# Performance work log

Measured on AMD Instinct MI355X. Metric: run time of the kernel, lower is better.

Reference implementation:

```python
import jax, jax.numpy as jnp
import numpy as np

WINDOW = 16  # signature_window_size
D = 6        # input_path_dim


def _mlp(x, Ws, bs, final_act):
    for W, b in zip(Ws[:-1], bs[:-1]):
        x = jax.nn.softplus(W @ x + b)
    return final_act(Ws[-1] @ x + bs[-1])


def _windowed_logsig(xs):
    """Depth-2 log-signature of each window of the (piecewise-linear) path.
    Returns level-1 increments [n, D] and Levy areas [n, D, D] (antisymmetric)."""
    dx = xs[1:] - xs[:-1]                              # [T-1, D]
    n = dx.shape[0] // WINDOW
    dxw = dx[: n * WINDOW].reshape(n, WINDOW, D)
    lvl1 = dxw.sum(axis=1)                             # [n, D]
    cum = jnp.cumsum(dxw, axis=1) - dxw                # exclusive prefix sums
    cross = jnp.einsum('nwi,nwj->nij', cum, dxw)
    area = 0.5 * (cross - jnp.swapaxes(cross, 1, 2))   # [n, D, D]
    return lvl1, area


def setup_inputs() -> dict:
    key = jax.random.key(0)
    ks = jax.random.split(key, 9)
    S, H, OUT = 128, 128, 10
    B, T = 8, 513

    def lin(k, o, i):
        return jax.random.normal(k, (o, i), jnp.float32) / np.sqrt(i)

    return {
        'x': jax.random.normal(ks[0], (B, T, D), jnp.float32),
        'W_i0': lin(ks[1], H, D), 'b_i0': jnp.zeros((H,), jnp.float32),
        'W_i1': lin(ks[2], H, H), 'b_i1': jnp.zeros((H,), jnp.float32),
        'W_i2': lin(ks[3], S, H), 'b_i2': jnp.zeros((S,), jnp.float32),
        'W_v0': lin(ks[4], H, S), 'b_v0': jnp.zeros((H,), jnp.float32),
        'W_v1': lin(ks[5], H, H), 'b_v1': jnp.zeros((H,), jnp.float32),
        'W_v2': lin(ks[6], D * S, H), 'b_v2': jnp.zeros((D * S,), jnp.float32),
        'W_r': lin(ks[7], OUT, S), 'b_r': jnp.zeros((OUT,), jnp.float32),
    }


def reference(x, W_i0, b_i0, W_i1, b_i1, W_i2, b_i2,
              W_v0, b_v0, W_v1, b_v1, W_v2, b_v2, W_r, b_r):
    S = W_i2.shape[0]
    init_mlp = lambda z: _mlp(z, (W_i0, W_i1, W_i2), (b_i0, b_i1, b_i2), lambda u: u)
    # Vector fields V_i: R^S -> R^S, one per input channel (split_multi_vector_field)
    vf = lambda h: _mlp(h, (W_v0, W_v1, W_v2), (b_v0, b_v1, b_v2), jnp.tanh).reshape(D, S)
    mask = jnp.triu(jnp.ones((D, D), x.dtype), 1)  # Lyndon words i<j at depth 2

    def single(xs):  # xs: [T, D]
        lvl1, area = _windowed_logsig(xs)
        h0 = init_mlp(xs[0])

        def step(h, sig):
            l1, a = sig
            V = vf(h)                                  # [D, S]
            J = jax.jacfwd(vf)(h)                      # [D, S, S], J[j,b,a]=dV_j[b]/dh[a]
            M = jnp.einsum('jba,ia->ijb', J, V)        # (DV_j)(h) V_i(h)
            brack = M - jnp.swapaxes(M, 0, 1)          # Lie brackets [V_i, V_j](h)
            h_new = h + jnp.einsum('i,ib->b', l1, V) \
                      + jnp.einsum('ij,ijb->b', a * mask, brack)  # log-ODE step
            return h_new, h_new

        _, hist = jax.lax.scan(step, h0, (lvl1, area))
        hist = jnp.concatenate([h0[None], hist], axis=0)   # [n+1, S]
        return hist @ W_r.T + b_r                          # evolving readout

    return jax.vmap(single)(x)
```

## Files before the change

kernel.cpp:

```cpp
#include <hip/hip_runtime.h>
#include <math.h>

#define D    6
#define S    128
#define H    128
#define WIN  16
#define BB   8
#define TT   513
#define NW   32
#define OUTD 10

__device__ float g_lvl1[BB * NW * D];
__device__ float g_area[BB * NW * D * D];
__device__ float g_h0[BB * S];
__device__ float g_hist[BB * (NW + 1) * S];

__device__ __forceinline__ float sp(float x) {
    return (x > 20.f) ? x : log1pf(expf(x));
}
__device__ __forceinline__ float sigm(float x) {
    return 1.f / (1.f + expf(-x));
}
__device__ __forceinline__ float dot4(float4 a, float4 b, float acc) {
    return fmaf(a.x, b.x, fmaf(a.y, b.y, fmaf(a.z, b.z, fmaf(a.w, b.w, acc))));
}

#define O_W0   0
#define O_W1   16384
#define O_PS   32768
#define O_U    35840
#define O_T    36608
#define O_V    37376
#define O_H    38144
#define O_U1   38400
#define O_U2   38528
#define O_SG1  38656
#define O_SG2  38784
#define O_B0   38912
#define O_B1   39040
#define O_SIG  39168
#define SMTOT  39256

__global__ __launch_bounds__(256) void k_sig(
        const float* __restrict__ x,
        const float* __restrict__ Wi0, const float* __restrict__ bi0,
        const float* __restrict__ Wi1, const float* __restrict__ bi1,
        const float* __restrict__ Wi2, const float* __restrict__ bi2) {
    const int b = blockIdx.x;
    const int tid = threadIdx.x;
    __shared__ float dxs[NW][WIN][D];
    __shared__ float cums[NW][WIN][D];
    __shared__ float ua[H], ub[H];

    const float* xb = x + (size_t)b * TT * D;

    if (tid < NW * D) {
        int w = tid / D, i = tid % D;
        float run = 0.f;
        float prev = xb[(w * WIN) * D + i];
        for (int k = 0; k < WIN; ++k) {
            float cur = xb[(w * WIN + k + 1) * D + i];
            float d = cur - prev; prev = cur;
            dxs[w][k][i] = d;
            cums[w][k][i] = run;
            run += d;
        }
        g_lvl1[(b * NW + w) * D + i] = run;
    }
    __syncthreads();
    for (int e = tid; e < NW * D * D; e += blockDim.x) {
        int w = e / (D * D); int rem = e % (D * D);
        int i = rem / D, j = rem % D;
        float s = 0.f;
        for (int k = 0; k < WIN; ++k)
            s += cums[w][k][i] * dxs[w][k][j] - cums[w][k][j] * dxs[w][k][i];
        g_area[(b * NW + w) * (D * D) + rem] = 0.5f * s;
    }
    if (tid < H) {
        float z = bi0[tid];
        for (int k = 0; k < D; ++k) z += Wi0[tid * D + k] * xb[k];
        ua[tid] = sp(z);
    }
    __syncthreads();
    if (tid < H) {
        float z = bi1[tid];
        for (int k = 0; k < H; ++k) z += Wi1[tid * H + k] * ua[k];
        ub[tid] = sp(z);
    }
    __syncthreads();
    if (tid < H) {
        float z = bi2[tid];
        for (int k = 0; k < H; ++k) z += Wi2[tid * H + k] * ub[k];
        g_h0[b * S + tid] = z;
    }
}

#define FOR16(X) X(0) X(1) X(2) X(3) X(4) X(5) X(6) X(7) \
                 X(8) X(9) X(10) X(11) X(12) X(13) X(14) X(15)
#define DECL_ABC(q) float4 wA##q, wB##q, wC##q;
#define LOAD_ABC(q) wA##q = W24[baseA + q]; wB##q = W24[baseB + q]; wC##q = W24[baseC + q];
#define S3_Q(q) { float4 u = U24[q]; \
    acc0 = dot4(wA##q, u, acc0); acc1 = dot4(wB##q, u, acc1); acc2 = dot4(wC##q, u, acc2); }
#define S6_Q(q) { \
    acc0 = dot4(wA##q, TA[q], acc0); acc1 = dot4(wB##q, TB[q], acc1); acc2 = dot4(wC##q, TC[q], acc2); }

__global__ __launch_bounds__(512, 2) void k_scan(
        const float* __restrict__ bv0, const float* __restrict__ bv1,
        const float* __restrict__ bv2,
        const float* __restrict__ Wv0, const float* __restrict__ Wv1,
        const float* __restrict__ Wv2) {
    __shared__ float sm[SMTOT];
    const int b = blockIdx.x, tid = threadIdx.x;
    const int r   = tid & 127;
    const int c4  = tid >> 7;
    const int key = r & 7;
    const int kh = tid & 1;
    const int r0 = tid >> 1, r1 = r0 + 256, r2 = r0 + 512;
    const int jA = tid >> 8, jB = 2 + jA, jC = 4 + jA;

    {
        float4* d = (float4*)(sm + O_W0);
        const float4* s0 = (const float4*)Wv0;
        const float4* s1 = (const float4*)Wv1;
        for (int i = tid; i < 4096; i += 512) { d[i] = s0[i]; d[4096 + i] = s1[i]; }
    }
    FOR16(DECL_ABC)
    const float4* W24 = (const float4*)Wv2;
    const int baseA = r0 * 32 + kh * 16;
    const int baseB = r1 * 32 + kh * 16;
    const int baseC = r2 * 32 + kh * 16;
    FOR16(LOAD_ABC)
    if (tid < 128) {
        sm[O_B0 + tid] = bv0[tid]; sm[O_B1 + tid] = bv1[tid];
        float h0v = g_h0[b * 128 + tid];
        sm[O_H + tid] = h0v;
        g_hist[(b * (NW + 1)) * 128 + tid] = h0v;
    }
    if (tid >= 448) {
        int q = tid - 448;
        if (q < 42)
            sm[O_SIG + q] = (q < 6) ? g_lvl1[(b * NW) * 6 + q]
                                    : g_area[(b * NW) * 36 + q - 6];
    }
    __syncthreads();

    const float4* W04 = (const float4*)(sm + O_W0);
    const float4* W14 = (const float4*)(sm + O_W1);

    int p = 0;
    for (int t = 0; t < NW; ++t) {
        float rsig = 0.f;
        if (tid >= 448) {
            int q = tid - 448;
            if (q < 42 && t + 1 < NW)
                rsig = (q < 6) ? g_lvl1[(b * NW + t + 1) * 6 + q]
                               : g_area[(b * NW + t + 1) * 36 + q - 6];
        }
        const int sb = O_SIG + (t & 1) * 44;

        {
            float a = 0.f;
            const float4* H4 = (const float4*)(sm + O_H + p * 128);
            #pragma unroll
            for (int q = 0; q < 8; ++q) {
                int qq = c4 * 8 + (q ^ key);
                a = dot4(W04[r * 32 + qq], H4[qq], a);
            }
            sm[O_PS + (c4 * 6) * 128 + r] = a;
        }
        __syncthreads();
        if (tid < 128) {
            float z = sm[O_B0 + tid];
            #pragma unroll
            for (int c = 0; c < 4; ++c) z += sm[O_PS + (c * 6) * 128 + tid];
            sm[O_U1 + tid] = sp(z); sm[O_SG1 + tid] = sigm(z);
        }
        __syncthreads();
        {
            float a = 0.f;
            const float4* U14 = (const float4*)(sm + O_U1);
            #pragma unroll
            for (int q = 0; q < 8; ++q) {
                int qq = c4 * 8 + (q ^ key);
                a = dot4(W14[r * 32 + qq], U14[qq], a);
            }
            sm[O_PS + (c4 * 6) * 128 + r] = a;
        }
        __syncthreads();
        if (tid < 128) {
            float z = sm[O_B1 + tid];
            #pragma unroll
            for (int c = 0; c < 4; ++c) z += sm[O_PS + (c * 6) * 128 + tid];
            sm[O_U2 + tid] = sp(z); sm[O_SG2 + tid] = sigm(z);
        }
        __syncthreads();
        {
            float acc0 = 0.f, acc1 = 0.f, acc2 = 0.f;
            const float4* U24 = (const float4*)(sm + O_U2) + kh * 16;
            FOR16(S3_Q)
            sm[O_PS + kh * 768 + r0] = acc0;
            sm[O_PS + kh * 768 + r1] = acc1;
            sm[O_PS + kh * 768 + r2] = acc2;
        }
        __syncthreads();
        {
            sm[O_V + tid] = tanhf(bv2[tid] + sm[O_PS + tid] + sm[O_PS + 768 + tid]);
            if (tid < 256) {
                int e = tid + 512;
                sm[O_V + e] = tanhf(bv2[e] + sm[O_PS + e] + sm[O_PS + 768 + e]);
            }
        }
        __syncthreads();
        {
            #pragma unroll
            for (int s = 0; s < 2; ++s) {
                int e = tid + s * 512;
                if (s == 0 || tid < 256) {
                    int jj = e >> 7, rr = e & 127;
                    float u = 0.f;
                    #pragma unroll
                    for (int i = 0; i < 6; ++i)
                        u = fmaf(sm[sb + 6 + i * 6 + jj], sm[O_V + i * 128 + rr], u);
                    sm[O_U + jj * 128 + rr] = u;
                }
            }
            if (tid < 128) {
                float xh = sm[O_H + p * 128 + tid];
                #pragma unroll
                for (int i = 0; i < 6; ++i)
                    xh = fmaf(sm[sb + i], sm[O_V + i * 128 + tid], xh);
                sm[O_H + (p ^ 1) * 128 + tid] = xh;
            }
        }
        __syncthreads();
        {
            float a0 = 0.f, a1 = 0.f, a2 = 0.f, a3 = 0.f, a4 = 0.f, a5 = 0.f;
            const float4* U4 = (const float4*)(sm + O_U);
            #pragma unroll
            for (int q = 0; q < 8; ++q) {
                int qq = c4 * 8 + (q ^ key);
                float4 w = W04[r * 32 + qq];
                a0 = dot4(w, U4[qq], a0);
                a1 = dot4(w, U4[32 + qq], a1);
                a2 = dot4(w, U4[64 + qq], a2);
                a3 = dot4(w, U4[96 + qq], a3);
                a4 = dot4(w, U4[128 + qq], a4);
                a5 = dot4(w, U4[160 + qq], a5);
            }
            sm[O_PS + (c4 * 6 + 0) * 128 + r] = a0;
            sm[O_PS + (c4 * 6 + 1) * 128 + r] = a1;
            sm[O_PS + (c4 * 6 + 2) * 128 + r] = a2;
            sm[O_PS + (c4 * 6 + 3) * 128 + r] = a3;
            sm[O_PS + (c4 * 6 + 4) * 128 + r] = a4;
            sm[O_PS + (c4 * 6 + 5) * 128 + r] = a5;
        }
        __syncthreads();
        {
            #pragma unroll
            for (int s = 0; s < 2; ++s) {
                int e = tid + s * 512;
                if (s == 0 || tid < 256) {
                    int jj = e >> 7, rr = e & 127;
                    float sv = sm[O_PS + jj * 128 + rr] + sm[O_PS + (6 + jj) * 128 + rr]
                             + sm[O_PS + (12 + jj) * 128 + rr] + sm[O_PS + (18 + jj) * 128 + rr];
                    sm[O_T + jj * 128 + rr] = sm[O_SG1 + rr] * sv;
                }
            }
        }
        __syncthreads();
        {
            float a0 = 0.f, a1 = 0.f, a2 = 0.f, a3 = 0.f, a4 = 0.f, a5 = 0.f;
            const float4* T4 = (const float4*)(sm + O_T);
            #pragma unroll
            for (int q = 0; q < 8; ++q) {
                int qq = c4 * 8 + (q ^ key);
                float4 w = W14[r * 32 + qq];
                a0 = dot4(w, T4[qq], a0);
                a1 = dot4(w, T4[32 + qq], a1);
                a2 = dot4(w, T4[64 + qq], a2);
                a3 = dot4(w, T4[96 + qq], a3);
                a4 = dot4(w, T4[128 + qq], a4);
                a5 = dot4(w, T4[160 + qq], a5);
            }
            sm[O_PS + (c4 * 6 + 0) * 128 + r] = a0;
            sm[O_PS + (c4 * 6 + 1) * 128 + r] = a1;
            sm[O_PS + (c4 * 6 + 2) * 128 + r] = a2;
            sm[O_PS + (c4 * 6 + 3) * 128 + r] = a3;
            sm[O_PS + (c4 * 6 + 4) * 128 + r] = a4;
            sm[O_PS + (c4 * 6 + 5) * 128 + r] = a5;
        }
        __syncthreads();
        {
            #pragma unroll
            for (int s = 0; s < 2; ++s) {
                int e = tid + s * 512;
                if (s == 0 || tid < 256) {
                    int jj = e >> 7, rr = e & 127;
                    float sv = sm[O_PS + jj * 128 + rr] + sm[O_PS + (6 + jj) * 128 + rr]
                             + sm[O_PS + (12 + jj) * 128 + rr] + sm[O_PS + (18 + jj) * 128 + rr];
                    sm[O_U + jj * 128 + rr] = sm[O_SG2 + rr] * sv;
                }
            }
        }
        __syncthreads();
        {
            float acc0 = 0.f, acc1 = 0.f, acc2 = 0.f;
            const float4* TA = (const float4*)(sm + O_U) + jA * 32 + kh * 16;
            const float4* TB = (const float4*)(sm + O_U) + jB * 32 + kh * 16;
            const float4* TC = (const float4*)(sm + O_U) + jC * 32 + kh * 16;
            FOR16(S6_Q)
            sm[O_PS + kh * 768 + r0] = acc0;
            sm[O_PS + kh * 768 + r1] = acc1;
            sm[O_PS + kh * 768 + r2] = acc2;
        }
        __syncthreads();
        {
            float v = sm[O_V + tid];
            sm[O_T + tid] = (1.f - v * v) * (sm[O_PS + tid] + sm[O_PS + 768 + tid]);
            if (tid < 256) {
                int e = tid + 512;
                float v2 = sm[O_V + e];
                sm[O_T + e] = (1.f - v2 * v2) * (sm[O_PS + e] + sm[O_PS + 768 + e]);
            }
        }
        __syncthreads();
        if (tid < 128) {
            float xh = sm[O_H + (p ^ 1) * 128 + tid];
            #pragma unroll
            for (int j = 0; j < 6; ++j) xh += sm[O_T + j * 128 + tid];
            sm[O_H + (p ^ 1) * 128 + tid] = xh;
            g_hist[(b * (NW + 1) + t + 1) * 128 + tid] = xh;
        }
        if (tid >= 448) {
            int q = tid - 448;
            if (q < 42 && t + 1 < NW)
                sm[O_SIG + ((t + 1) & 1) * 44 + q] = rsig;
        }
        p ^= 1;
        __syncthreads();
    }
}

__global__ __launch_bounds__(384) void k_read(const float* __restrict__ Wr,
                                              const float* __restrict__ br,
                                              float* __restrict__ out) {
    const int b = blockIdx.x, e = threadIdx.x;
    if (e < (NW + 1) * OUTD) {
        int t = e / OUTD, o = e % OUTD;
        float z = br[o];
        const float4* hrow = (const float4*)&g_hist[(b * (NW + 1) + t) * 128];
        const float4* wrow = (const float4*)&Wr[o * 128];
        float z0 = 0, z1 = 0, z2 = 0, z3 = 0;
        #pragma unroll 8
        for (int s4 = 0; s4 < 32; ++s4) {
            float4 hv = hrow[s4]; float4 wv = wrow[s4];
            z0 = fmaf(hv.x, wv.x, z0); z1 = fmaf(hv.y, wv.y, z1);
            z2 = fmaf(hv.z, wv.z, z2); z3 = fmaf(hv.w, wv.w, z3);
        }
        out[(b * (NW + 1) + t) * OUTD + o] = z + ((z0 + z1) + (z2 + z3));
    }
}

extern "C" void kernel_launch(void* const* d_in, const int* in_sizes, int n_in,
                              void* d_out, int out_size, void* d_ws, size_t ws_size,
                              hipStream_t stream) {
    const float* x   = (const float*)d_in[0];
    const float* Wi0 = (const float*)d_in[1];
    const float* bi0 = (const float*)d_in[2];
    const float* Wi1 = (const float*)d_in[3];
    const float* bi1 = (const float*)d_in[4];
    const float* Wi2 = (const float*)d_in[5];
    const float* bi2 = (const float*)d_in[6];
    const float* Wv0 = (const float*)d_in[7];
    const float* bv0 = (const float*)d_in[8];
    const float* Wv1 = (const float*)d_in[9];
    const float* bv1 = (const float*)d_in[10];
    const float* Wv2 = (const float*)d_in[11];
    const float* bv2 = (const float*)d_in[12];
    const float* Wr  = (const float*)d_in[13];
    const float* br  = (const float*)d_in[14];
    float* out = (float*)d_out;

    hipLaunchKernelGGL(k_sig,  dim3(BB), dim3(256), 0, stream,
                       x, Wi0, bi0, Wi1, bi1, Wi2, bi2);
    hipLaunchKernelGGL(k_scan, dim3(BB), dim3(512), 0, stream,
                       bv0, bv1, bv2, Wv0, Wv1, Wv2);
    hipLaunchKernelGGL(k_read, dim3(BB), dim3(384), 0, stream, Wr, br, out);
}
```

Before: 476.5 us.

## Replace shared-memory partial sums with wavefront shuffle reductions to cut barriers in scan

Reworks the per-step matvecs in the scan kernel so each output row is reduced across 4 or 2 adjacent lanes with shuffles instead of writing partials to shared memory and reducing in a separate phase. This removes about five barrier-separated phases per time step and fuses the activations (softplus/sigmoid/tanh, tanh derivative) into the reduction epilogue. Two-thirds of the Wv2 register cache is dropped in favour of global/L2 reads each step, and launch bounds no longer request 2 blocks per CU. The tradeoff is extra global loads for Wv2 rows in exchange for lower register pressure and fewer syncs.

```diff
diff --git a/kernel.cpp b/kernel.cpp
--- a/kernel.cpp
+++ b/kernel.cpp
@@ -27,19 +27,19 @@
 
 #define O_W0   0
 #define O_W1   16384
-#define O_PS   32768
-#define O_U    35840
-#define O_T    36608
-#define O_V    37376
-#define O_H    38144
-#define O_U1   38400
-#define O_U2   38528
-#define O_SG1  38656
-#define O_SG2  38784
-#define O_B0   38912
-#define O_B1   39040
-#define O_SIG  39168
-#define SMTOT  39256
+#define O_U1   32768
+#define O_SG1  32896
+#define O_U2   33024
+#define O_SG2  33152
+#define O_V    33280
+#define O_U    34048
+#define O_TB   34816
+#define O_H    35584
+#define O_B0   35840
+#define O_B1   35968
+#define O_B2   36096
+#define O_SIG  36864
+#define SMTOT  36952
 
 __global__ __launch_bounds__(256) void k_sig(
         const float* __restrict__ x,
@@ -97,39 +97,50 @@
 
 #define FOR16(X) X(0) X(1) X(2) X(3) X(4) X(5) X(6) X(7) \
                  X(8) X(9) X(10) X(11) X(12) X(13) X(14) X(15)
-#define DECL_ABC(q) float4 wA##q, wB##q, wC##q;
-#define LOAD_ABC(q) wA##q = W24[baseA + q]; wB##q = W24[baseB + q]; wC##q = W24[baseC + q];
-#define S3_Q(q) { float4 u = U24[q]; \
-    acc0 = dot4(wA##q, u, acc0); acc1 = dot4(wB##q, u, acc1); acc2 = dot4(wC##q, u, acc2); }
-#define S6_Q(q) { \
-    acc0 = dot4(wA##q, TA[q], acc0); acc1 = dot4(wB##q, TB[q], acc1); acc2 = dot4(wC##q, TC[q], acc2); }
-
-__global__ __launch_bounds__(512, 2) void k_scan(
+#define DECL_A(q) float4 wA##q;
+#define LOAD_A(q) wA##q = W24[baseA + q];
+#define C_Q(q) { float4 u = U24[q]; \
+    acc0 = dot4(wA##q, u, acc0); \
+    acc1 = dot4(Wm1[q], u, acc1); \
+    acc2 = dot4(Wm2[q], u, acc2); }
+#define G_Q(q) { \
+    acc0 = dot4(wA##q, TA[q], acc0); \
+    acc1 = dot4(Wm1[q], TJB[q], acc1); \
+    acc2 = dot4(Wm2[q], TJC[q], acc2); }
+
+__global__ __launch_bounds__(512) void k_scan(
         const float* __restrict__ bv0, const float* __restrict__ bv1,
         const float* __restrict__ bv2,
         const float* __restrict__ Wv0, const float* __restrict__ Wv1,
         const float* __restrict__ Wv2) {
     __shared__ float sm[SMTOT];
     const int b = blockIdx.x, tid = threadIdx.x;
-    const int r   = tid & 127;
-    const int c4  = tid >> 7;
-    const int key = r & 7;
+    const int r   = tid >> 2;
+    const int sub = tid & 3;
+    const int keyA = r & 7;
     const int kh = tid & 1;
-    const int r0 = tid >> 1, r1 = r0 + 256, r2 = r0 + 512;
-    const int jA = tid >> 8, jB = 2 + jA, jC = 4 + jA;
+    const int m  = tid >> 1;
+    const int rp = tid >> 3, jg = (tid >> 2) & 1, kq = tid & 3;
+    const int ra = 2 * rp, rb = ra + 1, j0 = 3 * jg;
+    const int keyE = rp & 7;
 
     {
         float4* d = (float4*)(sm + O_W0);
         const float4* s0 = (const float4*)Wv0;
         const float4* s1 = (const float4*)Wv1;
-        for (int i = tid; i < 4096; i += 512) { d[i] = s0[i]; d[4096 + i] = s1[i]; }
-    }
-    FOR16(DECL_ABC)
+        #pragma unroll
+        for (int i = 0; i < 8; ++i) { d[tid + i * 512] = s0[tid + i * 512]; }
+        #pragma unroll
+        for (int i = 0; i < 8; ++i) { d[4096 + tid + i * 512] = s1[tid + i * 512]; }
+        sm[O_B2 + tid] = bv2[tid];
+        if (tid < 256) sm[O_B2 + 512 + tid] = bv2[512 + tid];
+    }
+    FOR16(DECL_A)
     const float4* W24 = (const float4*)Wv2;
-    const int baseA = r0 * 32 + kh * 16;
-    const int baseB = r1 * 32 + kh * 16;
-    const int baseC = r2 * 32 + kh * 16;
-    FOR16(LOAD_ABC)
+    const int baseA = m * 32 + kh * 16;
+    FOR16(LOAD_A)
+    const float4* Wm1 = W24 + (m + 256) * 32 + kh * 16;
+    const float4* Wm2 = W24 + (m + 512) * 32 + kh * 16;
     if (tid < 128) {
         sm[O_B0 + tid] = bv0[tid]; sm[O_B1 + tid] = bv1[tid];
         float h0v = g_h0[b * 128 + tid];
@@ -159,55 +170,51 @@
         const int sb = O_SIG + (t & 1) * 44;
 
         {
-            float a = 0.f;
+            float a0 = 0.f, a1 = 0.f;
             const float4* H4 = (const float4*)(sm + O_H + p * 128);
             #pragma unroll
-            for (int q = 0; q < 8; ++q) {
-                int qq = c4 * 8 + (q ^ key);
-                a = dot4(W04[r * 32 + qq], H4[qq], a);
-            }
-            sm[O_PS + (c4 * 6) * 128 + r] = a;
-        }
-        __syncthreads();
-        if (tid < 128) {
-            float z = sm[O_B0 + tid];
-            #pragma unroll
-            for (int c = 0; c < 4; ++c) z += sm[O_PS + (c * 6) * 128 + tid];
-            sm[O_U1 + tid] = sp(z); sm[O_SG1 + tid] = sigm(z);
-        }
-        __syncthreads();
-        {
-            float a = 0.f;
+            for (int q = 0; q < 8; q += 2) {
+                int q0 = sub * 8 + (q ^ keyA);
+                int q1 = sub * 8 + ((q + 1) ^ keyA);
+                a0 = dot4(W04[r * 32 + q0], H4[q0], a0);
+                a1 = dot4(W04[r * 32 + q1], H4[q1], a1);
+            }
+            float tot = a0 + a1;
+            tot += __shfl_xor(tot, 1);
+            tot += __shfl_xor(tot, 2);
+            if (sub == 0)      sm[O_U1 + r]  = sp(sm[O_B0 + r] + tot);
+            else if (sub == 1) sm[O_SG1 + r] = sigm(sm[O_B0 + r] + tot);
+        }
+        __syncthreads();
+        {
+            float a0 = 0.f, a1 = 0.f;
             const float4* U14 = (const float4*)(sm + O_U1);
             #pragma unroll
-            for (int q = 0; q < 8; ++q) {
-                int qq = c4 * 8 + (q ^ key);
-                a = dot4(W14[r * 32 + qq], U14[qq], a);
-            }
-            sm[O_PS + (c4 * 6) * 128 + r] = a;
-        }
-        __syncthreads();
-        if (tid < 128) {
-            float z = sm[O_B1 + tid];
-            #pragma unroll
-            for (int c = 0; c < 4; ++c) z += sm[O_PS + (c * 6) * 128 + tid];
-            sm[O_U2 + tid] = sp(z); sm[O_SG2 + tid] = sigm(z);
+            for (int q = 0; q < 8; q += 2) {
+                int q0 = sub * 8 + (q ^ keyA);
+                int q1 = sub * 8 + ((q + 1) ^ keyA);
+                a0 = dot4(W14[r * 32 + q0], U14[q0], a0);
+                a1 = dot4(W14[r * 32 + q1], U14[q1], a1);
+            }
+            float tot = a0 + a1;
+            tot += __shfl_xor(tot, 1);
+            tot += __shfl_xor(tot, 2);
+            if (sub == 0)      sm[O_U2 + r]  = sp(sm[O_B1 + r] + tot);
+            else if (sub == 1) sm[O_SG2 + r] = sigm(sm[O_B1 + r] + tot);
         }
         __syncthreads();
         {
             float acc0 = 0.f, acc1 = 0.f, acc2 = 0.f;
             const float4* U24 = (const float4*)(sm + O_U2) + kh * 16;
-            FOR16(S3_Q)
-            sm[O_PS + kh * 768 + r0] = acc0;
-            sm[O_PS + kh * 768 + r1] = acc1;
-            sm[O_PS + kh * 768 + r2] = acc2;
-        }
-        __syncthreads();
-        {
-            sm[O_V + tid] = tanhf(bv2[tid] + sm[O_PS + tid] + sm[O_PS + 768 + tid]);
-            if (tid < 256) {
-                int e = tid + 512;
-                sm[O_V + e] = tanhf(bv2[e] + sm[O_PS + e] + sm[O_PS + 768 + e]);
+            FOR16(C_Q)
+            acc0 += __shfl_xor(acc0, 1);
+            acc1 += __shfl_xor(acc1, 1);
+            acc2 += __shfl_xor(acc2, 1);
+            if (kh == 0) {
+                sm[O_V + m]       = tanhf(sm[O_B2 + m] + acc0);
+                sm[O_V + m + 256] = tanhf(sm[O_B2 + m + 256] + acc1);
+            } else {
+                sm[O_V + m + 512] = tanhf(sm[O_B2 + m + 512] + acc2);
             }
         }
         __syncthreads();
@@ -234,100 +241,90 @@
         }
         __syncthreads();
         {
-            float a0 = 0.f, a1 = 0.f, a2 = 0.f, a3 = 0.f, a4 = 0.f, a5 = 0.f;
+            float aa0=0,aa1=0,aa2=0, ab0=0,ab1=0,ab2=0;
             const float4* U4 = (const float4*)(sm + O_U);
             #pragma unroll
             for (int q = 0; q < 8; ++q) {
-                int qq = c4 * 8 + (q ^ key);
-                float4 w = W04[r * 32 + qq];
-                a0 = dot4(w, U4[qq], a0);
-                a1 = dot4(w, U4[32 + qq], a1);
-                a2 = dot4(w, U4[64 + qq], a2);
-                a3 = dot4(w, U4[96 + qq], a3);
-                a4 = dot4(w, U4[128 + qq], a4);
-                a5 = dot4(w, U4[160 + qq], a5);
-            }
-            sm[O_PS + (c4 * 6 + 0) * 128 + r] = a0;
-            sm[O_PS + (c4 * 6 + 1) * 128 + r] = a1;
-            sm[O_PS + (c4 * 6 + 2) * 128 + r] = a2;
-            sm[O_PS + (c4 * 6 + 3) * 128 + r] = a3;
-            sm[O_PS + (c4 * 6 + 4) * 128 + r] = a4;
-            sm[O_PS + (c4 * 6 + 5) * 128 + r] = a5;
-        }
-        __syncthreads();
-        {
-            #pragma unroll
-            for (int s = 0; s < 2; ++s) {
-                int e = tid + s * 512;
-                if (s == 0 || tid < 256) {
-                    int jj = e >> 7, rr = e & 127;
-                    float sv = sm[O_PS + jj * 128 + rr] + sm[O_PS + (6 + jj) * 128 + rr]
-                             + sm[O_PS + (12 + jj) * 128 + rr] + sm[O_PS + (18 + jj) * 128 + rr];
-                    sm[O_T + jj * 128 + rr] = sm[O_SG1 + rr] * sv;
-                }
-            }
-        }
-        __syncthreads();
-        {
-            float a0 = 0.f, a1 = 0.f, a2 = 0.f, a3 = 0.f, a4 = 0.f, a5 = 0.f;
-            const float4* T4 = (const float4*)(sm + O_T);
+                int qq = kq * 8 + (q ^ keyE);
+                float4 wa = W04[ra * 32 + qq], wb = W04[rb * 32 + qq];
+                float4 u0 = U4[j0 * 32 + qq], u1 = U4[(j0+1) * 32 + qq], u2 = U4[(j0+2) * 32 + qq];
+                aa0 = dot4(wa, u0, aa0); aa1 = dot4(wa, u1, aa1); aa2 = dot4(wa, u2, aa2);
+                ab0 = dot4(wb, u0, ab0); ab1 = dot4(wb, u1, ab1); ab2 = dot4(wb, u2, ab2);
+            }
+            aa0 += __shfl_xor(aa0,1); aa0 += __shfl_xor(aa0,2);
+            aa1 += __shfl_xor(aa1,1); aa1 += __shfl_xor(aa1,2);
+            aa2 += __shfl_xor(aa2,1); aa2 += __shfl_xor(aa2,2);
+            ab0 += __shfl_xor(ab0,1); ab0 += __shfl_xor(ab0,2);
+            ab1 += __shfl_xor(ab1,1); ab1 += __shfl_xor(ab1,2);
+            ab2 += __shfl_xor(ab2,1); ab2 += __shfl_xor(ab2,2);
+            if (kq == 0) {
+                float sg = sm[O_SG1 + ra];
+                sm[O_TB + j0 * 128 + ra] = sg * aa0;
+                sm[O_TB + (j0+1) * 128 + ra] = sg * aa1;
+                sm[O_TB + (j0+2) * 128 + ra] = sg * aa2;
+            } else if (kq == 1) {
+                float sg = sm[O_SG1 + rb];
+                sm[O_TB + j0 * 128 + rb] = sg * ab0;
+                sm[O_TB + (j0+1) * 128 + rb] = sg * ab1;
+                sm[O_TB + (j0+2) * 128 + rb] = sg * ab2;
+            }
+        }
+        __syncthreads();
+        {
+            float aa0=0,aa1=0,aa2=0, ab0=0,ab1=0,ab2=0;
+            const float4* T4 = (const float4*)(sm + O_TB);
             #pragma unroll
             for (int q = 0; q < 8; ++q) {
-                int qq = c4 * 8 + (q ^ key);
-                float4 w = W14[r * 32 + qq];
-                a0 = dot4(w, T4[qq], a0);
-                a1 = dot4(w, T4[32 + qq], a1);
-                a2 = dot4(w, T4[64 + qq], a2);
-                a3 = dot4(w, T4[96 + qq], a3);
-                a4 = dot4(w, T4[128 + qq], a4);
-                a5 = dot4(w, T4[160 + qq], a5);
-            }
-            sm[O_PS + (c4 * 6 + 0) * 128 + r] = a0;
-            sm[O_PS + (c4 * 6 + 1) * 128 + r] = a1;
-            sm[O_PS + (c4 * 6 + 2) * 128 + r] = a2;
-            sm[O_PS + (c4 * 6 + 3) * 128 + r] = a3;
-            sm[O_PS + (c4 * 6 + 4) * 128 + r] = a4;
-            sm[O_PS + (c4 * 6 + 5) * 128 + r] = a5;
-        }
-        __syncthreads();
-        {
-            #pragma unroll
-            for (int s = 0; s < 2; ++s) {
-                int e = tid + s * 512;
-                if (s == 0 || tid < 256) {
-                    int jj = e >> 7, rr = e & 127;
-                    float sv = sm[O_PS + jj * 128 + rr] + sm[O_PS + (6 + jj) * 128 + rr]
-                             + sm[O_PS + (12 + jj) * 128 + rr] + sm[O_PS + (18 + jj) * 128 + rr];
-                    sm[O_U + jj * 128 + rr] = sm[O_SG2 + rr] * sv;
-                }
+                int qq = kq * 8 + (q ^ keyE);
+                float4 wa = W14[ra * 32 + qq], wb = W14[rb * 32 + qq];
+                float4 u0 = T4[j0 * 32 + qq], u1 = T4[(j0+1) * 32 + qq], u2 = T4[(j0+2) * 32 + qq];
+                aa0 = dot4(wa, u0, aa0); aa1 = dot4(wa, u1, aa1); aa2 = dot4(wa, u2, aa2);
+                ab0 = dot4(wb, u0, ab0); ab1 = dot4(wb, u1, ab1); ab2 = dot4(wb, u2, ab2);
+            }
+            aa0 += __shfl_xor(aa0,1); aa0 += __shfl_xor(aa0,2);
+            aa1 += __shfl_xor(aa1,1); aa1 += __shfl_xor(aa1,2);
+            aa2 += __shfl_xor(aa2,1); aa2 += __shfl_xor(aa2,2);
+            ab0 += __shfl_xor(ab0,1); ab0 += __shfl_xor(ab0,2);
+            ab1 += __shfl_xor(ab1,1); ab1 += __shfl_xor(ab1,2);
+            ab2 += __shfl_xor(ab2,1); ab2 += __shfl_xor(ab2,2);
+            if (kq == 0) {
+                float sg = sm[O_SG2 + ra];
+                sm[O_U + j0 * 128 + ra] = sg * aa0;
+                sm[O_U + (j0+1) * 128 + ra] = sg * aa1;
+                sm[O_U + (j0+2) * 128 + ra] = sg * aa2;
+            } else if (kq == 1) {
+                float sg = sm[O_SG2 + rb];
+                sm[O_U + j0 * 128 + rb] = sg * ab0;
+                sm[O_U + (j0+1) * 128 + rb] = sg * ab1;
+                sm[O_U + (j0+2) * 128 + rb] = sg * ab2;
             }
         }
         __syncthreads();
         {
             float acc0 = 0.f, acc1 = 0.f, acc2 = 0.f;
-            const float4* TA = (const float4*)(sm + O_U) + jA * 32 + kh * 16;
-            const float4* TB = (const float4*)(sm + O_U) + jB * 32 + kh * 16;
-            const float4* TC = (const float4*)(sm + O_U) + jC * 32 + kh * 16;
-            FOR16(S6_Q)
-            sm[O_PS + kh * 768 + r0] = acc0;
-            sm[O_PS + kh * 768 + r1] = acc1;
-            sm[O_PS + kh * 768 + r2] = acc2;
-        }
-        __syncthreads();
-        {
-            float v = sm[O_V + tid];
-            sm[O_T + tid] = (1.f - v * v) * (sm[O_PS + tid] + sm[O_PS + 768 + tid]);
-            if (tid < 256) {
-                int e = tid + 512;
-                float v2 = sm[O_V + e];
-                sm[O_T + e] = (1.f - v2 * v2) * (sm[O_PS + e] + sm[O_PS + 768 + e]);
+            const int jA = m >> 7;
+            const float4* TA  = (const float4*)(sm + O_U) + jA * 32 + kh * 16;
+            const float4* TJB = (const float4*)(sm + O_U) + (2 + jA) * 32 + kh * 16;
+            const float4* TJC = (const float4*)(sm + O_U) + (4 + jA) * 32 + kh * 16;
+            FOR16(G_Q)
+            acc0 += __shfl_xor(acc0, 1);
+            acc1 += __shfl_xor(acc1, 1);
+            acc2 += __shfl_xor(acc2, 1);
+            if (kh == 0) {
+                float v0 = sm[O_V + m];
+                float v1 = sm[O_V + m + 256];
+                sm[O_TB + m]       = (1.f - v0 * v0) * acc0;
+                sm[O_TB + m + 256] = (1.f - v1 * v1) * acc1;
+            } else {
+                float v2 = sm[O_V + m + 512];
+                sm[O_TB + m + 512] = (1.f - v2 * v2) * acc2;
             }
         }
         __syncthreads();
         if (tid < 128) {
             float xh = sm[O_H + (p ^ 1) * 128 + tid];
             #pragma unroll
-            for (int j = 0; j < 6; ++j) xh += sm[O_T + j * 128 + tid];
+            for (int j = 0; j < 6; ++j) xh += sm[O_TB + j * 128 + tid];
             sm[O_H + (p ^ 1) * 128 + tid] = xh;
             g_hist[(b * (NW + 1) + t + 1) * 128 + tid] = xh;
         }
```

After: 491.2 us. 1.03x slower.
